# Kernel optimization log

Measured on AMD Instinct MI355X. Metric: run time of the kernel, lower is better.

The kernel has to match this reference:

```python
import jax, jax.numpy as jnp
import numpy as np

B, T, M, D, K, L = 128, 50, 4, 64, 64, 16  # batch, seq len, num_beh, embed dim, num_classes, capsule_length
NUM_ITEMS = 100000
R_ITERS = 3


def _dyn_gru(x, C, Wx, bx, Wh, bh):
    """Dynamic capsule GRU. x: [B,M,T,D], C: [B,M,T,K,L] (routing state modulates update gate).
    Returns final hidden beh_e [B,M,K,L] and per-step candidate states beh_N [B,M,T,K,L]."""
    # precompute input projections for all steps: [B,M,T,3,K,L]
    gi = (jnp.einsum('bmtd,mdg->bmtg', x, Wx) + bx[:, None, :]).reshape(x.shape[0], M, T, 3, K, L)

    def step(h, inp):
        gi_t, C_t = inp  # gi_t: [B,M,3,K,L], C_t: [B,M,K,L]
        gh = (jnp.einsum('bmkl,mklg->bmkg', h, Wh) + bh).reshape(h.shape[0], M, K, 3, L)
        r = jax.nn.sigmoid(gi_t[:, :, 0] + gh[:, :, :, 0])
        z = jax.nn.sigmoid(gi_t[:, :, 1] + gh[:, :, :, 1] + C_t)  # dynamic gate via routing state C
        n = jnp.tanh(gi_t[:, :, 2] + r * gh[:, :, :, 2])
        h_new = (1.0 - z) * n + z * h
        return h_new, n

    h0 = jnp.zeros((x.shape[0], M, K, L), x.dtype)
    h_fin, ns = jax.lax.scan(step, h0, (jnp.moveaxis(gi, 2, 0), jnp.moveaxis(C, 2, 0)))
    return h_fin, jnp.moveaxis(ns, 0, 2)


def setup_inputs() -> dict:
    key = jax.random.key(0)
    ks = jax.random.split(key, 9)
    names = ['purchase_seq', 'cart_seq', 'fav_seq', 'click_seq']
    seqs = {n: jax.random.randint(k, (B, T), 0, NUM_ITEMS + 1) for n, k in zip(names, ks[:4])}
    item_emb = jax.random.normal(ks[4], (NUM_ITEMS + 1, D), jnp.float32) * 0.02
    item_emb = item_emb.at[0].set(0.0)  # padding_idx=0
    W = 0.01 * jax.random.uniform(ks[5], (K, L, M, K), jnp.float32)
    W_coef = 0.1 * jax.random.normal(ks[6], (K, D + L, L), jnp.float32)
    alpha = jnp.ones((1,), jnp.float32) * K
    w = jnp.ones((K,), jnp.float32)
    bias = jnp.zeros((K,), jnp.float32)
    gru_Wx = 0.05 * jax.random.normal(ks[7], (M, D, 3 * K * L), jnp.float32)
    gru_bx = jnp.zeros((M, 3 * K * L), jnp.float32)
    gru_Wh = 0.05 * jax.random.normal(ks[8], (M, K, L, 3 * L), jnp.float32)
    gru_bh = jnp.zeros((M, K, 3 * L), jnp.float32)
    return dict(**seqs, item_emb=item_emb, W=W, W_coef=W_coef, alpha=alpha, w=w, bias=bias,
                gru_Wx=gru_Wx, gru_bx=gru_bx, gru_Wh=gru_Wh, gru_bh=gru_bh)


def reference(purchase_seq, cart_seq, fav_seq, click_seq, item_emb, W, W_coef,
              alpha, w, bias, gru_Wx, gru_bx, gru_Wh, gru_bh):
    sg = jax.lax.stop_gradient

    def embed(seq):
        mask = (seq != 0).astype(item_emb.dtype)[..., None]
        return item_emb[seq] * mask

    x = jnp.stack([embed(purchase_seq), embed(cart_seq), embed(fav_seq), embed(click_seq)], axis=1)  # [B,M,T,D]
    bsz = x.shape[0]
    b = jnp.zeros((bsz, K, K, 1), x.dtype)
    C = jnp.zeros((bsz, M, T, K, L), x.dtype)

    # routing iterations (all GRU outputs / W / alpha / w / bias / item_emb detached; W_coef live)
    for _ in range(R_ITERS - 1):
        beh_e, beh_N = _dyn_gru(sg(x), sg(C), sg(gru_Wx), sg(gru_bx), sg(gru_Wh), sg(gru_bh))
        beh_e = sg(beh_e).transpose(0, 2, 1, 3)  # [B,K,M,L]
        u = jnp.einsum('bctd,cdtC->bcCd', beh_e, sg(W))  # [B,K,K,L]
        c = jax.nn.softmax(b, axis=2)
        v = sg(alpha) * jnp.sum(c * u, axis=1)  # [B,K,L]
        v_ = jnp.linalg.norm(v, axis=-1) * sg(w) + sg(bias)  # [B,K]
        E = sg(item_emb)
        p = jax.nn.softmax(v_ @ E.T, axis=-1) @ E  # [B,D]
        p = jnp.broadcast_to(p[:, None, :], (bsz, K, D))
        r = jnp.einsum('bcd,cdD->bcD', jnp.concatenate([p, v], axis=-1), W_coef)  # [B,K,L]
        b = b + jnp.sum(u * r[:, None], axis=-1, keepdims=True)
        C = C + sg(beh_N) * r[:, None, None]

    beh_e, _ = _dyn_gru(x, C, gru_Wx, gru_bx, gru_Wh, gru_bh)
    beh_e = beh_e.transpose(0, 2, 1, 3)
    u_hat = jnp.einsum('bctd,cdtC->bcCd', beh_e, W)
    c = jax.nn.softmax(b, axis=2)
    v = alpha * jnp.sum(c * u_hat, axis=1)
    v_ = jnp.linalg.norm(v, axis=-1) * w + bias
    return v_ @ item_emb.T  # [B, num_items+1]
```

## Files before the change

### kernel.cpp

```cpp
#include <hip/hip_runtime.h>
#include <hip/hip_bf16.h>
#include <cstdint>
#include <cstddef>

#define B_   128
#define T_   50
#define M_   4
#define D_   64
#define K_   64
#define L_   16
#define NIT  100001
#define NBP3 256
#define CHUNK3 391
#define PSTRIDE 8320

typedef unsigned short u16;
typedef unsigned int   u32;
typedef __attribute__((ext_vector_type(8))) short short8;
typedef __attribute__((ext_vector_type(4))) float f32x4;

__device__ __forceinline__ float bf2f(u16 v){ u32 u = ((u32)v)<<16; float f; __builtin_memcpy(&f,&u,4); return f; }
__device__ __forceinline__ u16 f2bf(float f){
  u32 u; __builtin_memcpy(&u,&f,4);
  u32 r = (u + 0x7FFFu + ((u>>16)&1u)) >> 16;
  return (u16)r;
}
__device__ __forceinline__ float fexp(float x){ return __builtin_amdgcn_exp2f(x*1.4426950408889634f); }
__device__ __forceinline__ float fsig(float x){ return __builtin_amdgcn_rcpf(1.0f + fexp(-x)); }
__device__ __forceinline__ float ftanh(float x){ return 1.0f - 2.0f*__builtin_amdgcn_rcpf(1.0f + fexp(2.0f*x)); }
__device__ __forceinline__ void unpack8(const u32* s, short8& h, short8& l){
  #pragma unroll
  for (int q=0;q<8;q++){ h[q]=(short)(s[q]&0xFFFFu); l[q]=(short)(s[q]>>16); }
}

__global__ __launch_bounds__(256) void k_prep_x(const int* __restrict__ s0, const int* __restrict__ s1,
  const int* __restrict__ s2, const int* __restrict__ s3, const float* __restrict__ E,
  u16* __restrict__ xh, u16* __restrict__ xl)
{
  int id = blockIdx.x*256 + threadIdx.x;
  int e8 = id & 7;
  int rm = id >> 3;
  int m = rm / 6400; int r = rm - m*6400;
  int t = r >> 7, b = r & 127;
  const int* sq = (m==0)? s0 : (m==1)? s1 : (m==2)? s2 : s3;
  int idx = sq[b*T_ + t];
  float sc = (idx==0)? 0.0f : 1.0f;
  const float4* ep = (const float4*)(E + (size_t)idx*64 + e8*8);
  float4 v0 = ep[0], v1 = ep[1];
  float vals[8] = {v0.x,v0.y,v0.z,v0.w,v1.x,v1.y,v1.z,v1.w};
  u32 hw[4], lw[4];
  #pragma unroll
  for (int q=0;q<4;q++){
    float f0 = vals[2*q]*sc, f1 = vals[2*q+1]*sc;
    u16 h0 = f2bf(f0), h1 = f2bf(f1);
    u16 l0 = f2bf(f0 - bf2f(h0)), l1 = f2bf(f1 - bf2f(h1));
    hw[q] = (u32)h0 | ((u32)h1<<16);
    lw[q] = (u32)l0 | ((u32)l1<<16);
  }
  size_t off = (size_t)rm*64 + e8*8;
  uint4 hv; hv.x=hw[0]; hv.y=hw[1]; hv.z=hw[2]; hv.w=hw[3];
  uint4 lv; lv.x=lw[0]; lv.y=lw[1]; lv.z=lw[2]; lv.w=lw[3];
  *(uint4*)(xh + off) = hv;
  *(uint4*)(xl + off) = lv;
}

__global__ __launch_bounds__(256) void k_prep_w(const float* __restrict__ Wx,
  u16* __restrict__ wh, u16* __restrict__ wl)
{
  __shared__ float tl[64][65];
  int m = blockIdx.x / 48, gt = blockIdx.x % 48;
  for (int it=0; it<16; ++it){
    int li = threadIdx.x + it*256;
    int dl = li >> 6, gl = li & 63;
    tl[dl][gl] = Wx[((size_t)m*64 + dl)*3072 + gt*64 + gl];
  }
  __syncthreads();
  for (int it=0; it<2; ++it){
    int unit = threadIdx.x + it*256;
    int gl = unit >> 3, d8 = unit & 7;
    u32 hw[4], lw[4];
    #pragma unroll
    for (int q=0;q<4;q++){
      float f0 = tl[d8*8+2*q][gl], f1 = tl[d8*8+2*q+1][gl];
      u16 h0 = f2bf(f0), h1 = f2bf(f1);
      u16 l0 = f2bf(f0 - bf2f(h0)), l1 = f2bf(f1 - bf2f(h1));
      hw[q] = (u32)h0 | ((u32)h1<<16);
      lw[q] = (u32)l0 | ((u32)l1<<16);
    }
    size_t off = ((size_t)m*3072 + gt*64 + gl)*64 + d8*8;
    uint4 hv; hv.x=hw[0]; hv.y=hw[1]; hv.z=hw[2]; hv.w=hw[3];
    uint4 lv; lv.x=lw[0]; lv.y=lw[1]; lv.z=lw[2]; lv.w=lw[3];
    *(uint4*)(wh + off) = hv;
    *(uint4*)(wl + off) = lv;
  }
}

__global__ __launch_bounds__(256) void k_gemm_gi(const u16* __restrict__ xh, const u16* __restrict__ xl,
  const u16* __restrict__ wh, const u16* __restrict__ wl,
  const float* __restrict__ bx, const float* __restrict__ bhp, u16* __restrict__ gi)
{
  int bi = blockIdx.x;
  int q4 = bi & 3; int k = (bi>>2)&63; int m = bi>>8;
  int wv = threadIdx.x>>6, lane = threadIdx.x&63;
  int n16 = lane & 15, quad = lane >> 4;

  short8 Ah[3][2], Al[3][2];
  #pragma unroll
  for (int gate=0; gate<3; ++gate){
    int g = gate*1024 + k*16 + n16;
    #pragma unroll
    for (int c=0; c<2; ++c){
      size_t aoff = ((size_t)(m*3072 + g))*64 + c*32 + quad*8;
      Ah[gate][c] = *(const short8*)(wh + aoff);
      Al[gate][c] = *(const short8*)(wl + aoff);
    }
  }
  float bias[3][4];
  #pragma unroll
  for (int gate=0; gate<3; ++gate){
    #pragma unroll
    for (int rg=0; rg<4; ++rg){
      int j = quad*4 + rg;
      int g = gate*1024 + k*16 + j;
      bias[gate][rg] = bx[m*3072 + g] + ((gate<2)? bhp[(m*64+k)*48 + gate*16 + j] : 0.0f);
    }
  }
  for (int i=0; i<25; ++i){
    int row = q4*1600 + (i*4+wv)*16 + n16;
    size_t xoff = ((size_t)(m*6400 + row))*64 + quad*8;
    short8 Bh0 = *(const short8*)(xh + xoff);
    short8 Bh1 = *(const short8*)(xh + xoff + 32);
    short8 Bl0 = *(const short8*)(xl + xoff);
    short8 Bl1 = *(const short8*)(xl + xoff + 32);
    #pragma unroll
    for (int gate=0; gate<3; ++gate){
      f32x4 acc = {bias[gate][0], bias[gate][1], bias[gate][2], bias[gate][3]};
      acc = __builtin_amdgcn_mfma_f32_16x16x32_bf16(Ah[gate][0], Bh0, acc, 0,0,0);
      acc = __builtin_amdgcn_mfma_f32_16x16x32_bf16(Ah[gate][1], Bh1, acc, 0,0,0);
      acc = __builtin_amdgcn_mfma_f32_16x16x32_bf16(Al[gate][0], Bh0, acc, 0,0,0);
      acc = __builtin_amdgcn_mfma_f32_16x16x32_bf16(Al[gate][1], Bh1, acc, 0,0,0);
      acc = __builtin_amdgcn_mfma_f32_16x16x32_bf16(Ah[gate][0], Bl0, acc, 0,0,0);
      acc = __builtin_amdgcn_mfma_f32_16x16x32_bf16(Ah[gate][1], Bl1, acc, 0,0,0);
      u32 w0 = (u32)f2bf(acc[0]) | ((u32)f2bf(acc[1])<<16);
      u32 w1 = (u32)f2bf(acc[2]) | ((u32)f2bf(acc[3])<<16);
      size_t go = (((size_t)(m*64+k)*3 + gate)*6400 + row)*16 + quad*4;
      uint2 st; st.x = w0; st.y = w1;
      *(uint2*)(gi + go) = st;
    }
  }
}

template<int RC, int WN, int FOLD>
__global__ __launch_bounds__(256,4) void k_gru(u16* __restrict__ gi, const float* __restrict__ Wh,
  const float* __restrict__ bhp, const float* __restrict__ rp,
  u16* __restrict__ Nbuf, float* __restrict__ behE)
{
  __shared__ float hbuf[256];
  int tid = threadIdx.x;
  int wave = tid>>6, lane = tid&63;
  int bg = lane>>4, j = lane&15;
  int bi = blockIdx.x;
  int bblk = bi & 7; bi >>= 3;
  int k = bi & 63; int m = bi >> 6;
  int b = bblk*16 + wave*4 + bg;
  float wr[16], wz[16], wn[16];
  const float* whp = Wh + ((size_t)(m*64+k)*16)*48;
  #pragma unroll
  for (int l=0;l<16;l++){
    wr[l] = whp[l*48 + j];
    wz[l] = whp[l*48 + 16 + j];
    wn[l] = whp[l*48 + 32 + j];
  }
  float bhn = bhp[(m*64+k)*48 + 32 + j];
  float rv = 0.f;
  if (RC) rv = rp[((size_t)b*64+k)*16 + j];
  float hown = 0.0f;
  hbuf[tid] = 0.0f;
  __builtin_amdgcn_wave_barrier();
  size_t pbase = ((size_t)(m*64+k)*3)*102400 + b*16 + j;
  const u16* gR = gi + pbase;
  u16*       gZ = gi + pbase + 102400;
  const u16* gN = gi + pbase + 204800;
  u16*       nP = Nbuf + ((size_t)(m*64+k))*102400 + b*16 + j;
  const float* hgrp = &hbuf[tid & ~15];
  float gir_c = bf2f(gR[0]);
  float giz_c = bf2f(gZ[0]);
  float gin_c = bf2f(gN[0]);
  float Nc = 0.f;
  if (RC) Nc = bf2f(nP[0]);
  for (int t=0;t<50;++t){
    float gir_n=0.f, giz_n=0.f, gin_n=0.f, Nn=0.f;
    if (t<49){
      int nxt = (t+1)*2048;
      gir_n = bf2f(gR[nxt]);
      giz_n = bf2f(gZ[nxt]);
      gin_n = bf2f(gN[nxt]);
      if (RC) Nn = bf2f(nP[nxt]);
    }
    float Ct = 0.0f;
    if (RC) Ct = Nc * rv;
    if (FOLD) gZ[t*2048] = f2bf(giz_c + Ct);
    float hv[16];
    *(float4*)&hv[0]  = ((const float4*)hgrp)[0];
    *(float4*)&hv[4]  = ((const float4*)hgrp)[1];
    *(float4*)&hv[8]  = ((const float4*)hgrp)[2];
    *(float4*)&hv[12] = ((const float4*)hgrp)[3];
    float ghr = 0.f, ghz = 0.f, ghn = bhn;
    #pragma unroll
    for (int l=0;l<16;l++){ ghr += hv[l]*wr[l]; ghz += hv[l]*wz[l]; ghn += hv[l]*wn[l]; }
    float rg = fsig(gir_c + ghr);
    float zg = fsig(giz_c + ghz + Ct);
    float ng = ftanh(gin_c + rg*ghn);
    float hn = ng + zg*(hown - ng);
    if (WN) nP[t*2048] = f2bf(ng);
    hown = hn;
    __builtin_amdgcn_wave_barrier();
    hbuf[tid] = hn;
    __builtin_amdgcn_wave_barrier();
    gir_c=gir_n; giz_c=giz_n; gin_c=gin_n; Nc=Nn;
  }
  behE[(((size_t)b*64 + k)*4 + m)*16 + j] = hown;
}

__global__ __launch_bounds__(256) void k_cv(const float* __restrict__ bmat, const float* __restrict__ behE,
  const float* __restrict__ W, const float* __restrict__ alpha, const float* __restrict__ wv,
  const float* __restrict__ bias, float* __restrict__ vout, float* __restrict__ vT)
{
  __shared__ float cm[64][65];
  __shared__ float vsh[64][17];
  __shared__ float besh[4096];
  int b = blockIdx.x, tid = threadIdx.x;
  for (int it=0; it<16; ++it){
    int li = tid + it*256;
    cm[li>>6][li&63] = bmat[(size_t)b*4096 + li];
    besh[li] = behE[(size_t)b*4096 + li];
  }
  __syncthreads();
  if (tid < 64){
    float mx = -1e30f;
    for (int jj=0;jj<64;jj++) mx = fmaxf(mx, cm[tid][jj]);
    float sm = 0.f;
    for (int jj=0;jj<64;jj++){ float e = fexp(cm[tid][jj]-mx); cm[tid][jj]=e; sm+=e; }
    float inv = 1.0f/sm;
    for (int jj=0;jj<64;jj++) cm[tid][jj] *= inv;
  }
  __syncthreads();
  int j = tid & 63, dq = tid>>6;
  float a0=0,a1=0,a2=0,a3=0;
  for (int i=0;i<64;++i){
    float cij = cm[i][j];
    #pragma unroll
    for (int q=0;q<4;++q){
      int d = dq*4+q;
      const float* wp = W + ((size_t)((i*16+d)*4))*64 + j;
      float uu = besh[i*64+d]*wp[0] + besh[i*64+16+d]*wp[64]
               + besh[i*64+32+d]*wp[128] + besh[i*64+48+d]*wp[192];
      float cu = cij*uu;
      if (q==0) a0 += cu; else if (q==1) a1 += cu; else if (q==2) a2 += cu; else a3 += cu;
    }
  }
  float al = alpha[0];
  a0*=al; a1*=al; a2*=al; a3*=al;
  vsh[j][dq*4]=a0; vsh[j][dq*4+1]=a1; vsh[j][dq*4+2]=a2; vsh[j][dq*4+3]=a3;
  float* vp = vout + ((size_t)b*64 + j)*16 + dq*4;
  vp[0]=a0; vp[1]=a1; vp[2]=a2; vp[3]=a3;
  __syncthreads();
  if (tid < 64){
    float s=0.f;
    #pragma unroll
    for (int dd=0; dd<16; ++dd){ float q = vsh[tid][dd]; s += q*q; }
    vT[tid*128 + b] = sqrtf(s)*wv[tid] + bias[tid];
  }
}

__global__ __launch_bounds__(256) void k_prep_v(const float* __restrict__ vT, u32* __restrict__ vBp)
{
  int id = blockIdx.x*256 + threadIdx.x;
  int b = id>>6, c = id&63;
  float v = vT[c*128 + b];
  u16 h = f2bf(v); u16 l = f2bf(v - bf2f(h));
  vBp[id] = (u32)h | ((u32)l<<16);
}

__global__ __launch_bounds__(256) void k_pfused(const u32* __restrict__ vBp, const float* __restrict__ E,
  float* __restrict__ partial)
{
  __shared__ u16 etAh[32*72], etAl[32*72];
  __shared__ u16 etBh[64*32], etBl[64*32];
  __shared__ u32 exT[128*36];
  int tid = threadIdx.x, lane = tid&63, w = tid>>6;
  int n16 = lane&15, quad = lane>>4;

  short8 vh[2][2], vl[2][2];
  #pragma unroll
  for (int nt2=0; nt2<2; ++nt2){
    int b = (2*w+nt2)*16 + n16;
    #pragma unroll
    for (int s=0; s<2; ++s){
      u32 tmp[8];
      const u32* src = vBp + b*64 + s*32 + quad*8;
      #pragma unroll
      for (int q=0;q<8;q++) tmp[q]=src[q];
      unpack8(tmp, vh[nt2][s], vl[nt2][s]);
    }
  }
  f32x4 pacc[2][4];
  #pragma unroll
  for (int a2=0;a2<2;a2++)
    #pragma unroll
    for (int b2=0;b2<4;b2++){ pacc[a2][b2][0]=0.f; pacc[a2][b2][1]=0.f; pacc[a2][b2][2]=0.f; pacc[a2][b2][3]=0.f; }
  float srun[2] = {0.f, 0.f};

  int start = blockIdx.x*CHUNK3;
  int bend = start + CHUNK3; if (bend > NIT) bend = NIT;
  int sitem = tid>>3, sc0 = (tid&7)*8;
  for (int ch=0; ch<13; ++ch){
    int i0 = start + ch*32;
    if (i0 >= bend) break;
    {
      int gidx = i0 + sitem;
      float vals[8];
      if (gidx < NIT){
        float4 a = ((const float4*)E)[(size_t)gidx*16 + (sc0>>2)];
        float4 b2 = ((const float4*)E)[(size_t)gidx*16 + (sc0>>2) + 1];
        vals[0]=a.x; vals[1]=a.y; vals[2]=a.z; vals[3]=a.w;
        vals[4]=b2.x; vals[5]=b2.y; vals[6]=b2.z; vals[7]=b2.w;
      } else {
        #pragma unroll
        for (int q=0;q<8;q++) vals[q]=0.f;
      }
      u16 hh[8], ll[8];
      #pragma unroll
      for (int q=0;q<8;q++){ hh[q]=f2bf(vals[q]); ll[q]=f2bf(vals[q]-bf2f(hh[q])); }
      *(short8*)(etAh + sitem*72 + sc0) = *(short8*)hh;
      *(short8*)(etAl + sitem*72 + sc0) = *(short8*)ll;
      #pragma unroll
      for (int q=0;q<8;q++){
        etBh[(sc0+q)*32 + sitem] = hh[q];
        etBl[(sc0+q)*32 + sitem] = ll[q];
      }
    }
    __syncthreads();
    short8 Eh[2][2], El[2][2];
    #pragma unroll
    for (int mt=0; mt<2; ++mt)
      #pragma unroll
      for (int s=0; s<2; ++s){
        const u16* base = etAh + (mt*16 + n16)*72 + s*32 + quad*8;
        Eh[mt][s] = *(const short8*)base;
        El[mt][s] = *(const short8*)(base + 32*72);
      }
    #pragma unroll
    for (int mt=0; mt<2; ++mt)
      #pragma unroll
      for (int s=0; s<2; ++s)
        El[mt][s] = *(const short8*)(etAl + (mt*16 + n16)*72 + s*32 + quad*8);
    #pragma unroll
    for (int mt=0; mt<2; ++mt){
      #pragma unroll
      for (int nt2=0; nt2<2; ++nt2){
        f32x4 a = {0.f,0.f,0.f,0.f};
        #pragma unroll
        for (int s=0; s<2; ++s){
          a = __builtin_amdgcn_mfma_f32_16x16x32_bf16(Eh[mt][s], vh[nt2][s], a, 0,0,0);
          a = __builtin_amdgcn_mfma_f32_16x16x32_bf16(Eh[mt][s], vl[nt2][s], a, 0,0,0);
          a = __builtin_amdgcn_mfma_f32_16x16x32_bf16(El[mt][s], vh[nt2][s], a, 0,0,0);
        }
        u32 packed[4];
        #pragma unroll
        for (int rg=0; rg<4; ++rg){
          int it_g = i0 + mt*16 + quad*4 + rg;
          float ex = (it_g < bend)? fexp(a[rg]) : 0.f;
          srun[nt2] += ex;
          u16 h = f2bf(ex); u16 l = f2bf(ex - bf2f(h));
          packed[rg] = (u32)h | ((u32)l<<16);
        }
        int bl = (2*w+nt2)*16 + n16;
        uint4 st; st.x=packed[0]; st.y=packed[1]; st.z=packed[2]; st.w=packed[3];
        *(uint4*)(exT + bl*36 + mt*16 + quad*4) = st;
      }
    }
    __syncthreads();
    short8 Xh[2], Xl[2];
    #pragma unroll
    for (int mt2=0; mt2<2; ++mt2){
      int bl = (2*w+mt2)*16 + n16;
      uint4 t0 = *(const uint4*)(exT + bl*36 + quad*8);
      uint4 t1 = *(const uint4*)(exT + bl*36 + quad*8 + 4);
      u32 tmp[8] = {t0.x,t0.y,t0.z,t0.w,t1.x,t1.y,t1.z,t1.w};
      unpack8(tmp, Xh[mt2], Xl[mt2]);
    }
    #pragma unroll
    for (int nt3=0; nt3<4; ++nt3){
      int d = nt3*16 + n16;
      short8 Bh = *(const short8*)(etBh + d*32 + quad*8);
      short8 Bl = *(const short8*)(etBl + d*32 + quad*8);
      #pragma unroll
      for (int mt2=0; mt2<2; ++mt2){
        pacc[mt2][nt3] = __builtin_amdgcn_mfma_f32_16x16x32_bf16(Xh[mt2], Bh, pacc[mt2][nt3], 0,0,0);
        pacc[mt2][nt3] = __builtin_amdgcn_mfma_f32_16x16x32_bf16(Xh[mt2], Bl, pacc[mt2][nt3], 0,0,0);
        pacc[mt2][nt3] = __builtin_amdgcn_mfma_f32_16x16x32_bf16(Xl[mt2], Bh, pacc[mt2][nt3], 0,0,0);
      }
    }
    __syncthreads();
  }
  float* dst = partial + (size_t)blockIdx.x*PSTRIDE;
  #pragma unroll
  for (int mt2=0; mt2<2; ++mt2)
    #pragma unroll
    for (int nt3=0; nt3<4; ++nt3)
      #pragma unroll
      for (int rg=0; rg<4; ++rg){
        int b_g = (2*w+mt2)*16 + quad*4 + rg;
        int d_g = nt3*16 + n16;
        dst[b_g*64 + d_g] = pacc[mt2][nt3][rg];
      }
  #pragma unroll
  for (int nt2=0; nt2<2; ++nt2){
    float vsum = srun[nt2];
    vsum += __shfl_xor(vsum, 16);
    vsum += __shfl_xor(vsum, 32);
    if (quad == 0) dst[8192 + (2*w+nt2)*16 + n16] = vsum;
  }
}

__global__ __launch_bounds__(256) void k_pcomb(const float* __restrict__ partial, float* __restrict__ p)
{
  int id = blockIdx.x*256 + threadIdx.x;
  int b = id>>6;
  float a = 0.f, s = 0.f;
  for (int q=0;q<NBP3;q++){
    a += partial[(size_t)q*PSTRIDE + id];
    s += partial[(size_t)q*PSTRIDE + 8192 + b];
  }
  p[id] = a/s;
}

__global__ __launch_bounds__(256) void k_r(const float* __restrict__ p, const float* __restrict__ v,
  const float* __restrict__ Wc, float* __restrict__ r, float* __restrict__ rT)
{
  int gid = blockIdx.x*256 + threadIdx.x;
  int l = gid & 15, j = (gid>>4)&63, b = gid>>10;
  const float* wc = Wc + ((size_t)j*80)*16 + l;
  const float* pbp = p + b*64;
  float acc = 0.f;
  #pragma unroll 8
  for (int d=0; d<64; ++d) acc += pbp[d]*wc[d*16];
  const float* vb = v + ((size_t)b*64 + j)*16;
  #pragma unroll
  for (int d=0; d<16; ++d) acc += vb[d]*wc[(64+d)*16];
  r[((size_t)b*64+j)*16 + l] = acc;
  rT[((size_t)b*16+l)*64 + j] = acc;
}

__global__ __launch_bounds__(256) void k_bupd(const float* __restrict__ behE, const float* __restrict__ W,
  const float* __restrict__ rT, float* __restrict__ bmat)
{
  int lane = threadIdx.x & 63;
  int idx = blockIdx.x*4 + (threadIdx.x>>6);
  int b = idx >> 6, i = idx & 63;
  const float* be = behE + (size_t)idx*64;
  const float* rp = rT + (size_t)b*1024;
  float acc = 0.f;
  #pragma unroll
  for (int d=0; d<16; ++d){
    const float* wp = W + ((size_t)((i*16+d)*4))*64 + lane;
    float uu = be[d]*wp[0] + be[16+d]*wp[64] + be[32+d]*wp[128] + be[48+d]*wp[192];
    acc += uu * rp[d*64 + lane];
  }
  bmat[(size_t)idx*64 + lane] += acc;
}

__global__ __launch_bounds__(256) void k_logits(const u32* __restrict__ vBp, const float* __restrict__ E,
  float* __restrict__ out)
{
  __shared__ u16 etAh[64*72], etAl[64*72];
  __shared__ float lt[128*68];
  int tid = threadIdx.x, lane = tid&63, w = tid>>6;
  int n16 = lane&15, quad = lane>>4;
  short8 vh[2][2], vl[2][2];
  #pragma unroll
  for (int nt2=0; nt2<2; ++nt2){
    int b = (2*w+nt2)*16 + n16;
    #pragma unroll
    for (int s=0; s<2; ++s){
      u32 tmp[8];
      const u32* src = vBp + b*64 + s*32 + quad*8;
      #pragma unroll
      for (int q=0;q<8;q++) tmp[q]=src[q];
      unpack8(tmp, vh[nt2][s], vl[nt2][s]);
    }
  }
  int i0 = blockIdx.x*64;
  {
    int sitem = tid>>2, sc0 = (tid&3)*16;
    int gidx = i0 + sitem;
    float vals[16];
    if (gidx < NIT){
      #pragma unroll
      for (int q=0;q<4;q++){
        float4 a = ((const float4*)E)[(size_t)gidx*16 + (sc0>>2) + q];
        vals[4*q]=a.x; vals[4*q+1]=a.y; vals[4*q+2]=a.z; vals[4*q+3]=a.w;
      }
    } else {
      #pragma unroll
      for (int q=0;q<16;q++) vals[q]=0.f;
    }
    u16 hh[16], ll[16];
    #pragma unroll
    for (int q=0;q<16;q++){ hh[q]=f2bf(vals[q]); ll[q]=f2bf(vals[q]-bf2f(hh[q])); }
    *(short8*)(etAh + sitem*72 + sc0)     = *(short8*)hh;
    *(short8*)(etAh + sitem*72 + sc0 + 8) = *(short8*)(hh+8);
    *(short8*)(etAl + sitem*72 + sc0)     = *(short8*)ll;
    *(short8*)(etAl + sitem*72 + sc0 + 8) = *(short8*)(ll+8);
  }
  __syncthreads();
  #pragma unroll
  for (int mt=0; mt<4; ++mt){
    short8 Eh[2], El[2];
    #pragma unroll
    for (int s=0; s<2; ++s){
      Eh[s] = *(const short8*)(etAh + (mt*16 + n16)*72 + s*32 + quad*8);
      El[s] = *(const short8*)(etAl + (mt*16 + n16)*72 + s*32 + quad*8);
    }
    #pragma unroll
    for (int nt2=0; nt2<2; ++nt2){
      f32x4 a = {0.f,0.f,0.f,0.f};
      #pragma unroll
      for (int s=0; s<2; ++s){
        a = __builtin_amdgcn_mfma_f32_16x16x32_bf16(Eh[s], vh[nt2][s], a, 0,0,0);
        a = __builtin_amdgcn_mfma_f32_16x16x32_bf16(Eh[s], vl[nt2][s], a, 0,0,0);
        a = __builtin_amdgcn_mfma_f32_16x16x32_bf16(El[s], vh[nt2][s], a, 0,0,0);
      }
      int b = (2*w+nt2)*16 + n16;
      *(float4*)(lt + b*68 + mt*16 + quad*4) = *(float4*)&a;
    }
  }
  __syncthreads();
  int col = tid & 63, rgp = tid >> 6;
  if (i0 + col < NIT){
    #pragma unroll
    for (int rr=0; rr<32; ++rr){
      int b = rgp*32 + rr;
      out[(size_t)b*NIT + i0 + col] = lt[b*68 + col];
    }
  }
}

extern "C" void kernel_launch(void* const* d_in, const int* in_sizes, int n_in,
                              void* d_out, int out_size, void* d_ws, size_t ws_size,
                              hipStream_t stream)
{
  (void)in_sizes; (void)n_in; (void)out_size; (void)ws_size;
  const int*   s0 = (const int*)d_in[0];
  const int*   s1 = (const int*)d_in[1];
  const int*   s2 = (const int*)d_in[2];
  const int*   s3 = (const int*)d_in[3];
  const float* E  = (const float*)d_in[4];
  const float* W  = (const float*)d_in[5];
  const float* Wc = (const float*)d_in[6];
  const float* alpha = (const float*)d_in[7];
  const float* wv    = (const float*)d_in[8];
  const float* bias  = (const float*)d_in[9];
  const float* Wx = (const float*)d_in[10];
  const float* bx = (const float*)d_in[11];
  const float* Wh = (const float*)d_in[12];
  const float* bh = (const float*)d_in[13];

  char* ws = (char*)d_ws;
  size_t off = 0;
  auto alloc = [&](size_t bytes)->void*{ void* q = ws + off; off += (bytes + 255) & ~(size_t)255; return q; };
  u16*   gi   = (u16*)  alloc((size_t)M_*K_*T_*B_*48*2);
  u16*   N1   = (u16*)  alloc((size_t)M_*K_*T_*B_*16*2);
  u16*   xh   = (u16*)  alloc((size_t)M_*6400*64*2);
  u16*   xl   = (u16*)  alloc((size_t)M_*6400*64*2);
  u16*   wh   = (u16*)  alloc((size_t)M_*3072*64*2);
  u16*   wl   = (u16*)  alloc((size_t)M_*3072*64*2);
  float* bmat = (float*)alloc((size_t)B_*64*64*4);
  float* behE = (float*)alloc((size_t)B_*64*4*16*4);
  float* v    = (float*)alloc((size_t)B_*64*16*4);
  float* vT   = (float*)alloc((size_t)64*128*4);
  u32*   vBp  = (u32*)  alloc((size_t)128*64*4);
  float* r1   = (float*)alloc((size_t)B_*64*16*4);
  float* rT1  = (float*)alloc((size_t)B_*64*16*4);
  float* r2   = (float*)alloc((size_t)B_*64*16*4);
  float* rT2  = (float*)alloc((size_t)B_*64*16*4);
  float* p    = (float*)alloc((size_t)B_*64*4);
  float* partial = (float*)alloc((size_t)NBP3*PSTRIDE*4);

  hipMemsetAsync(bmat, 0, (size_t)B_*64*64*4, stream);
  k_prep_x<<<800,256,0,stream>>>(s0,s1,s2,s3,E,xh,xl);
  k_prep_w<<<192,256,0,stream>>>(Wx,wh,wl);
  k_gemm_gi<<<1024,256,0,stream>>>(xh,xl,wh,wl,bx,bh,gi);

  k_gru<0,1,0><<<2048,256,0,stream>>>(gi,Wh,bh,nullptr,N1,behE);
  k_cv<<<128,256,0,stream>>>(bmat,behE,W,alpha,wv,bias,v,vT);
  k_prep_v<<<32,256,0,stream>>>(vT,vBp);
  k_pfused<<<NBP3,256,0,stream>>>(vBp,E,partial);
  k_pcomb<<<32,256,0,stream>>>(partial,p);
  k_r<<<512,256,0,stream>>>(p,v,Wc,r1,rT1);
  k_bupd<<<2048,256,0,stream>>>(behE,W,rT1,bmat);

  k_gru<1,1,1><<<2048,256,0,stream>>>(gi,Wh,bh,r1,N1,behE);
  k_cv<<<128,256,0,stream>>>(bmat,behE,W,alpha,wv,bias,v,vT);
  k_prep_v<<<32,256,0,stream>>>(vT,vBp);
  k_pfused<<<NBP3,256,0,stream>>>(vBp,E,partial);
  k_pcomb<<<32,256,0,stream>>>(partial,p);
  k_r<<<512,256,0,stream>>>(p,v,Wc,r2,rT2);
  k_bupd<<<2048,256,0,stream>>>(behE,W,rT2,bmat);

  k_gru<1,0,0><<<2048,256,0,stream>>>(gi,Wh,bh,r2,N1,behE);
  k_cv<<<128,256,0,stream>>>(bmat,behE,W,alpha,wv,bias,v,vT);
  k_prep_v<<<32,256,0,stream>>>(vT,vBp);
  k_logits<<<1563,256,0,stream>>>(vBp,E,(float*)d_out);
}
```

Before: 572.7 us.

## Fuse input projection into GRU kernel and use MFMA for recurrent matmul

Removes the separate gi GEMM kernel and its large bf16 gi buffer, recomputing the input projection per timestep inside each GRU pass with MFMA. The recurrent h·Wh product moves from per-lane FMA loops over LDS-shared hidden state to split-bf16 16x16x16 MFMAs, with the hidden state kept in registers. The routing state C is rebuilt from separately stored N1/N2 buffers instead of being folded into gi. This trades gi memory traffic for recomputing the input GEMM three times, and adds bf16 split precision on the recurrence.

After: 513.5 us. -10.3%, faster.

```diff
diff --git a/kernel.cpp b/kernel.cpp
--- a/kernel.cpp
+++ b/kernel.cpp
@@ -17,6 +17,7 @@
 typedef unsigned short u16;
 typedef unsigned int   u32;
 typedef __attribute__((ext_vector_type(8))) short short8;
+typedef __attribute__((ext_vector_type(4))) short short4v;
 typedef __attribute__((ext_vector_type(4))) float f32x4;
 
 __device__ __forceinline__ float bf2f(u16 v){ u32 u = ((u32)v)<<16; float f; __builtin_memcpy(&f,&u,4); return f; }
@@ -32,6 +33,23 @@
   #pragma unroll
   for (int q=0;q<8;q++){ h[q]=(short)(s[q]&0xFFFFu); l[q]=(short)(s[q]>>16); }
 }
+
+#define MFMA32(A,Bv,C) __builtin_amdgcn_mfma_f32_16x16x32_bf16(A,Bv,C,0,0,0)
+
+#if __has_builtin(__builtin_amdgcn_mfma_f32_16x16x16bf16_1k)
+__device__ __forceinline__ f32x4 mfma16(short4v a, short4v b, f32x4 c){
+  return __builtin_amdgcn_mfma_f32_16x16x16bf16_1k(a,b,c,0,0,0);
+}
+#elif __has_builtin(__builtin_amdgcn_mfma_f32_16x16x16_bf16)
+__device__ __forceinline__ f32x4 mfma16(short4v a, short4v b, f32x4 c){
+  return __builtin_amdgcn_mfma_f32_16x16x16_bf16(a,b,c,0,0,0);
+}
+#else
+__device__ __forceinline__ f32x4 mfma16(short4v a, short4v b, f32x4 c){
+  asm("v_mfma_f32_16x16x16_bf16 %0, %1, %2, %0" : "+v"(c) : "v"(a), "v"(b));
+  return c;
+}
+#endif
 
 __global__ __launch_bounds__(256) void k_prep_x(const int* __restrict__ s0, const int* __restrict__ s1,
   const int* __restrict__ s2, const int* __restrict__ s3, const float* __restrict__ E,
@@ -95,131 +113,156 @@
   }
 }
 
-__global__ __launch_bounds__(256) void k_gemm_gi(const u16* __restrict__ xh, const u16* __restrict__ xl,
+template<int PASS>
+__global__ __launch_bounds__(256,2) void k_gru_mfma(
+  const u16* __restrict__ xh, const u16* __restrict__ xl,
   const u16* __restrict__ wh, const u16* __restrict__ wl,
-  const float* __restrict__ bx, const float* __restrict__ bhp, u16* __restrict__ gi)
-{
-  int bi = blockIdx.x;
-  int q4 = bi & 3; int k = (bi>>2)&63; int m = bi>>8;
-  int wv = threadIdx.x>>6, lane = threadIdx.x&63;
+  const float* __restrict__ Wh, const float* __restrict__ bx, const float* __restrict__ bhp,
+  const float* __restrict__ rp1, const float* __restrict__ rp2,
+  const u16* __restrict__ Nr1, const u16* __restrict__ Nr2,
+  u16* __restrict__ Nw, float* __restrict__ behE)
+{
+  int tid = threadIdx.x;
+  int lane = tid & 63;
   int n16 = lane & 15, quad = lane >> 4;
-
-  short8 Ah[3][2], Al[3][2];
-  #pragma unroll
-  for (int gate=0; gate<3; ++gate){
-    int g = gate*1024 + k*16 + n16;
+  int j0 = quad*4;
+  int wid = blockIdx.x*4 + (tid>>6);
+  int bt = wid & 7, k = (wid>>3)&63, m = wid>>9;
+  int b = bt*16 + n16;
+
+  short8 WxH[3][2], WxL[3][2];
+  #pragma unroll
+  for (int g=0; g<3; ++g){
+    int grow = g*1024 + k*16 + n16;
     #pragma unroll
     for (int c=0; c<2; ++c){
-      size_t aoff = ((size_t)(m*3072 + g))*64 + c*32 + quad*8;
-      Ah[gate][c] = *(const short8*)(wh + aoff);
-      Al[gate][c] = *(const short8*)(wl + aoff);
-    }
-  }
-  float bias[3][4];
-  #pragma unroll
-  for (int gate=0; gate<3; ++gate){
+      size_t off = ((size_t)(m*3072 + grow))*64 + c*32 + quad*8;
+      WxH[g][c] = *(const short8*)(wh + off);
+      WxL[g][c] = *(const short8*)(wl + off);
+    }
+  }
+  const float* whp = Wh + ((size_t)(m*64+k)*16)*48;
+  short4v WhH[3], WhL[3];
+  #pragma unroll
+  for (int g=0; g<3; ++g){
+    short4v hhv, llv;
+    #pragma unroll
+    for (int i=0;i<4;i++){
+      float w = whp[(j0+i)*48 + g*16 + n16];
+      u16 hbits = f2bf(w);
+      hhv[i] = (short)hbits;
+      llv[i] = (short)f2bf(w - bf2f(hbits));
+    }
+    WhH[g]=hhv; WhL[g]=llv;
+  }
+  float biasv[3][4], bhn[4];
+  #pragma unroll
+  for (int g=0; g<3; ++g)
     #pragma unroll
     for (int rg=0; rg<4; ++rg){
-      int j = quad*4 + rg;
-      int g = gate*1024 + k*16 + j;
-      bias[gate][rg] = bx[m*3072 + g] + ((gate<2)? bhp[(m*64+k)*48 + gate*16 + j] : 0.0f);
-    }
-  }
-  for (int i=0; i<25; ++i){
-    int row = q4*1600 + (i*4+wv)*16 + n16;
-    size_t xoff = ((size_t)(m*6400 + row))*64 + quad*8;
-    short8 Bh0 = *(const short8*)(xh + xoff);
-    short8 Bh1 = *(const short8*)(xh + xoff + 32);
-    short8 Bl0 = *(const short8*)(xl + xoff);
-    short8 Bl1 = *(const short8*)(xl + xoff + 32);
-    #pragma unroll
-    for (int gate=0; gate<3; ++gate){
-      f32x4 acc = {bias[gate][0], bias[gate][1], bias[gate][2], bias[gate][3]};
-      acc = __builtin_amdgcn_mfma_f32_16x16x32_bf16(Ah[gate][0], Bh0, acc, 0,0,0);
-      acc = __builtin_amdgcn_mfma_f32_16x16x32_bf16(Ah[gate][1], Bh1, acc, 0,0,0);
-      acc = __builtin_amdgcn_mfma_f32_16x16x32_bf16(Al[gate][0], Bh0, acc, 0,0,0);
-      acc = __builtin_amdgcn_mfma_f32_16x16x32_bf16(Al[gate][1], Bh1, acc, 0,0,0);
-      acc = __builtin_amdgcn_mfma_f32_16x16x32_bf16(Ah[gate][0], Bl0, acc, 0,0,0);
-      acc = __builtin_amdgcn_mfma_f32_16x16x32_bf16(Ah[gate][1], Bl1, acc, 0,0,0);
-      u32 w0 = (u32)f2bf(acc[0]) | ((u32)f2bf(acc[1])<<16);
-      u32 w1 = (u32)f2bf(acc[2]) | ((u32)f2bf(acc[3])<<16);
-      size_t go = (((size_t)(m*64+k)*3 + gate)*6400 + row)*16 + quad*4;
-      uint2 st; st.x = w0; st.y = w1;
-      *(uint2*)(gi + go) = st;
-    }
-  }
-}
-
-template<int RC, int WN, int FOLD>
-__global__ __launch_bounds__(256,4) void k_gru(u16* __restrict__ gi, const float* __restrict__ Wh,
-  const float* __restrict__ bhp, const float* __restrict__ rp,
-  u16* __restrict__ Nbuf, float* __restrict__ behE)
-{
-  __shared__ float hbuf[256];
-  int tid = threadIdx.x;
-  int wave = tid>>6, lane = tid&63;
-  int bg = lane>>4, j = lane&15;
-  int bi = blockIdx.x;
-  int bblk = bi & 7; bi >>= 3;
-  int k = bi & 63; int m = bi >> 6;
-  int b = bblk*16 + wave*4 + bg;
-  float wr[16], wz[16], wn[16];
-  const float* whp = Wh + ((size_t)(m*64+k)*16)*48;
-  #pragma unroll
-  for (int l=0;l<16;l++){
-    wr[l] = whp[l*48 + j];
-    wz[l] = whp[l*48 + 16 + j];
-    wn[l] = whp[l*48 + 32 + j];
-  }
-  float bhn = bhp[(m*64+k)*48 + 32 + j];
-  float rv = 0.f;
-  if (RC) rv = rp[((size_t)b*64+k)*16 + j];
-  float hown = 0.0f;
-  hbuf[tid] = 0.0f;
-  __builtin_amdgcn_wave_barrier();
-  size_t pbase = ((size_t)(m*64+k)*3)*102400 + b*16 + j;
-  const u16* gR = gi + pbase;
-  u16*       gZ = gi + pbase + 102400;
-  const u16* gN = gi + pbase + 204800;
-  u16*       nP = Nbuf + ((size_t)(m*64+k))*102400 + b*16 + j;
-  const float* hgrp = &hbuf[tid & ~15];
-  float gir_c = bf2f(gR[0]);
-  float giz_c = bf2f(gZ[0]);
-  float gin_c = bf2f(gN[0]);
-  float Nc = 0.f;
-  if (RC) Nc = bf2f(nP[0]);
+      int j = j0+rg;
+      float tb = bx[m*3072 + g*1024 + k*16 + j];
+      if (g<2) tb += bhp[(m*64+k)*48 + g*16 + j];
+      biasv[g][rg] = tb;
+    }
+  #pragma unroll
+  for (int rg=0; rg<4; ++rg) bhn[rg] = bhp[(m*64+k)*48 + 32 + j0 + rg];
+
+  float rv1[4]={0.f,0.f,0.f,0.f}, rv2[4]={0.f,0.f,0.f,0.f};
+  if (PASS>=2){
+    float4 q = *(const float4*)(rp1 + ((size_t)b*64+k)*16 + j0);
+    rv1[0]=q.x; rv1[1]=q.y; rv1[2]=q.z; rv1[3]=q.w;
+  }
+  if (PASS==3){
+    float4 q = *(const float4*)(rp2 + ((size_t)b*64+k)*16 + j0);
+    rv2[0]=q.x; rv2[1]=q.y; rv2[2]=q.z; rv2[3]=q.w;
+  }
+
+  size_t xrow  = ((size_t)m*6400 + bt*16 + n16)*64 + quad*8;
+  size_t nbase = ((size_t)(m*64+k))*102400 + (size_t)b*16 + j0;
+
+  short4v hH = {0,0,0,0}, hL = {0,0,0,0};
+  float hprev[4] = {0.f,0.f,0.f,0.f};
+
+  short8 cBh0 = *(const short8*)(xh + xrow);
+  short8 cBh1 = *(const short8*)(xh + xrow + 32);
+  short8 cBl0 = *(const short8*)(xl + xrow);
+  short8 cBl1 = *(const short8*)(xl + xrow + 32);
+  uint2 cN1 = {0,0}, cN2 = {0,0};
+  if (PASS>=2) cN1 = *(const uint2*)(Nr1 + nbase);
+  if (PASS==3) cN2 = *(const uint2*)(Nr2 + nbase);
+
   for (int t=0;t<50;++t){
-    float gir_n=0.f, giz_n=0.f, gin_n=0.f, Nn=0.f;
+    short8 nBh0, nBh1, nBl0, nBl1; uint2 nN1={0,0}, nN2={0,0};
     if (t<49){
-      int nxt = (t+1)*2048;
-      gir_n = bf2f(gR[nxt]);
-      giz_n = bf2f(gZ[nxt]);
-      gin_n = bf2f(gN[nxt]);
-      if (RC) Nn = bf2f(nP[nxt]);
-    }
-    float Ct = 0.0f;
-    if (RC) Ct = Nc * rv;
-    if (FOLD) gZ[t*2048] = f2bf(giz_c + Ct);
-    float hv[16];
-    *(float4*)&hv[0]  = ((const float4*)hgrp)[0];
-    *(float4*)&hv[4]  = ((const float4*)hgrp)[1];
-    *(float4*)&hv[8]  = ((const float4*)hgrp)[2];
-    *(float4*)&hv[12] = ((const float4*)hgrp)[3];
-    float ghr = 0.f, ghz = 0.f, ghn = bhn;
-    #pragma unroll
-    for (int l=0;l<16;l++){ ghr += hv[l]*wr[l]; ghz += hv[l]*wz[l]; ghn += hv[l]*wn[l]; }
-    float rg = fsig(gir_c + ghr);
-    float zg = fsig(giz_c + ghz + Ct);
-    float ng = ftanh(gin_c + rg*ghn);
-    float hn = ng + zg*(hown - ng);
-    if (WN) nP[t*2048] = f2bf(ng);
-    hown = hn;
-    __builtin_amdgcn_wave_barrier();
-    hbuf[tid] = hn;
-    __builtin_amdgcn_wave_barrier();
-    gir_c=gir_n; giz_c=giz_n; gin_c=gin_n; Nc=Nn;
-  }
-  behE[(((size_t)b*64 + k)*4 + m)*16 + j] = hown;
+      size_t xo = xrow + (size_t)(t+1)*8192;
+      nBh0 = *(const short8*)(xh + xo);
+      nBh1 = *(const short8*)(xh + xo + 32);
+      nBl0 = *(const short8*)(xl + xo);
+      nBl1 = *(const short8*)(xl + xo + 32);
+      if (PASS>=2) nN1 = *(const uint2*)(Nr1 + nbase + (size_t)(t+1)*2048);
+      if (PASS==3) nN2 = *(const uint2*)(Nr2 + nbase + (size_t)(t+1)*2048);
+    }
+    f32x4 giA[3];
+    #pragma unroll
+    for (int g=0; g<3; ++g){
+      f32x4 a = {biasv[g][0], biasv[g][1], biasv[g][2], biasv[g][3]};
+      a = MFMA32(WxH[g][0], cBh0, a);
+      a = MFMA32(WxH[g][1], cBh1, a);
+      a = MFMA32(WxL[g][0], cBh0, a);
+      a = MFMA32(WxL[g][1], cBh1, a);
+      a = MFMA32(WxH[g][0], cBl0, a);
+      a = MFMA32(WxH[g][1], cBl1, a);
+      giA[g] = a;
+    }
+    f32x4 ghr = {0.f,0.f,0.f,0.f};
+    f32x4 ghz = {0.f,0.f,0.f,0.f};
+    f32x4 ghn = {bhn[0], bhn[1], bhn[2], bhn[3]};
+    ghr = mfma16(WhH[0], hH, ghr); ghr = mfma16(WhL[0], hH, ghr); ghr = mfma16(WhH[0], hL, ghr);
+    ghz = mfma16(WhH[1], hH, ghz); ghz = mfma16(WhL[1], hH, ghz); ghz = mfma16(WhH[1], hL, ghz);
+    ghn = mfma16(WhH[2], hH, ghn); ghn = mfma16(WhL[2], hH, ghn); ghn = mfma16(WhH[2], hL, ghn);
+
+    u32 np0=0, np1=0;
+    short4v hHn = {0,0,0,0}, hLn = {0,0,0,0};
+    #pragma unroll
+    for (int rg=0; rg<4; ++rg){
+      float Ct = 0.f;
+      if (PASS>=2){
+        u32 wbits = (rg<2)? cN1.x : cN1.y;
+        Ct = bf2f((u16)(wbits >> ((rg&1)*16))) * rv1[rg];
+      }
+      if (PASS==3){
+        u32 wbits = (rg<2)? cN2.x : cN2.y;
+        Ct += bf2f((u16)(wbits >> ((rg&1)*16))) * rv2[rg];
+      }
+      float rr = fsig(giA[0][rg] + ghr[rg]);
+      float zz = fsig(giA[1][rg] + ghz[rg] + Ct);
+      float nn = ftanh(giA[2][rg] + rr*ghn[rg]);
+      float hv = nn + zz*(hprev[rg]-nn);
+      hprev[rg] = hv;
+      if (PASS<=2){
+        u32 nb = f2bf(nn);
+        if (rg==0) np0 |= nb;
+        else if (rg==1) np0 |= nb<<16;
+        else if (rg==2) np1 |= nb;
+        else np1 |= nb<<16;
+      }
+      u16 hb = f2bf(hv);
+      hHn[rg] = (short)hb;
+      hLn[rg] = (short)f2bf(hv - bf2f(hb));
+    }
+    if (PASS<=2){
+      uint2 st; st.x=np0; st.y=np1;
+      *(uint2*)(Nw + nbase + (size_t)t*2048) = st;
+    }
+    hH = hHn; hL = hLn;
+    if (t<49){
+      cBh0=nBh0; cBh1=nBh1; cBl0=nBl0; cBl1=nBl1;
+      cN1=nN1; cN2=nN2;
+    }
+  }
+  float4 st; st.x=hprev[0]; st.y=hprev[1]; st.z=hprev[2]; st.w=hprev[3];
+  *(float4*)(behE + (((size_t)b*64 + k)*4 + m)*16 + j0) = st;
 }
 
 __global__ __launch_bounds__(256) void k_cv(const float* __restrict__ bmat, const float* __restrict__ behE,
@@ -348,13 +391,8 @@
       for (int s=0; s<2; ++s){
         const u16* base = etAh + (mt*16 + n16)*72 + s*32 + quad*8;
         Eh[mt][s] = *(const short8*)base;
-        El[mt][s] = *(const short8*)(base + 32*72);
-      }
-    #pragma unroll
-    for (int mt=0; mt<2; ++mt)
-      #pragma unroll
-      for (int s=0; s<2; ++s)
         El[mt][s] = *(const short8*)(etAl + (mt*16 + n16)*72 + s*32 + quad*8);
+      }
     #pragma unroll
     for (int mt=0; mt<2; ++mt){
       #pragma unroll
@@ -570,8 +608,8 @@
   char* ws = (char*)d_ws;
   size_t off = 0;
   auto alloc = [&](size_t bytes)->void*{ void* q = ws + off; off += (bytes + 255) & ~(size_t)255; return q; };
-  u16*   gi   = (u16*)  alloc((size_t)M_*K_*T_*B_*48*2);
   u16*   N1   = (u16*)  alloc((size_t)M_*K_*T_*B_*16*2);
+  u16*   N2   = (u16*)  alloc((size_t)M_*K_*T_*B_*16*2);
   u16*   xh   = (u16*)  alloc((size_t)M_*6400*64*2);
   u16*   xl   = (u16*)  alloc((size_t)M_*6400*64*2);
   u16*   wh   = (u16*)  alloc((size_t)M_*3072*64*2);
@@ -591,9 +629,9 @@
   hipMemsetAsync(bmat, 0, (size_t)B_*64*64*4, stream);
   k_prep_x<<<800,256,0,stream>>>(s0,s1,s2,s3,E,xh,xl);
   k_prep_w<<<192,256,0,stream>>>(Wx,wh,wl);
-  k_gemm_gi<<<1024,256,0,stream>>>(xh,xl,wh,wl,bx,bh,gi);
-
-  k_gru<0,1,0><<<2048,256,0,stream>>>(gi,Wh,bh,nullptr,N1,behE);
+
+  k_gru_mfma<1><<<512,256,0,stream>>>(xh,xl,wh,wl,Wh,bx,bh,
+                                      nullptr,nullptr,nullptr,nullptr, N1, behE);
   k_cv<<<128,256,0,stream>>>(bmat,behE,W,alpha,wv,bias,v,vT);
   k_prep_v<<<32,256,0,stream>>>(vT,vBp);
   k_pfused<<<NBP3,256,0,stream>>>(vBp,E,partial);
@@ -601,7 +639,8 @@
   k_r<<<512,256,0,stream>>>(p,v,Wc,r1,rT1);
   k_bupd<<<2048,256,0,stream>>>(behE,W,rT1,bmat);
 
-  k_gru<1,1,1><<<2048,256,0,stream>>>(gi,Wh,bh,r1,N1,behE);
+  k_gru_mfma<2><<<512,256,0,stream>>>(xh,xl,wh,wl,Wh,bx,bh,
+                                      r1,nullptr, N1,nullptr, N2, behE);
   k_cv<<<128,256,0,stream>>>(bmat,behE,W,alpha,wv,bias,v,vT);
   k_prep_v<<<32,256,0,stream>>>(vT,vBp);
   k_pfused<<<NBP3,256,0,stream>>>(vBp,E,partial);
@@ -609,7 +648,8 @@
   k_r<<<512,256,0,stream>>>(p,v,Wc,r2,rT2);
   k_bupd<<<2048,256,0,stream>>>(behE,W,rT2,bmat);
 
-  k_gru<1,0,0><<<2048,256,0,stream>>>(gi,Wh,bh,r2,N1,behE);
+  k_gru_mfma<3><<<512,256,0,stream>>>(xh,xl,wh,wl,Wh,bx,bh,
+                                      r1,r2, N1,N2, nullptr, behE);
   k_cv<<<128,256,0,stream>>>(bmat,behE,W,alpha,wv,bias,v,vT);
   k_prep_v<<<32,256,0,stream>>>(vT,vBp);
   k_logits<<<1563,256,0,stream>>>(vBp,E,(float*)d_out);
```
